# Kernel tuning notes

Measured on AMD Instinct MI355X. Metric: run time of the kernel, lower is better.

Reference implementation:

```python
import jax, jax.numpy as jnp
import numpy as np

N_NODES = 50000
N_EDGES = 800000
IN_DIM = 64
OUT_DIM = 64
HID = OUT_DIM // 2  # 32
N_LAYERS = 9  # layer_num; layer_num >= 7 => no temporal conv, conv dropout unused


def _layernorm(x, w, b, eps=1e-5):
    mu = jnp.mean(x, axis=-1, keepdims=True)
    var = jnp.var(x, axis=-1, keepdims=True)
    return (x - mu) * jax.lax.rsqrt(var + eps) * w + b


def _conv(x, Wp, Wn, Ws, src, tgt, pos_m, neg_m):
    # relation-wise gather -> linear -> masked merge -> single scatter_add
    xs = x[src]  # [E, d_in]
    m = jnp.where(pos_m[:, None], xs @ Wp.T, 0.0) + jnp.where(neg_m[:, None], xs @ Wn.T, 0.0)
    agg = jax.ops.segment_sum(m, tgt, num_segments=N_NODES)
    return agg + x @ Ws.T


def _asfr(x, ln_w, ln_b, gw, gb):
    xn = _layernorm(x, ln_w, ln_b)
    w = jax.nn.sigmoid(xn @ gw.T + gb)
    w1 = jnp.where(w > 0.5, 1.0, w)
    w2 = jnp.where(w > 0.5, 0.0, w)
    x1 = w1 * x
    x2 = w2 * x
    h = x.shape[1] // 2
    return jnp.concatenate([x1[:, :h] + x2[:, h:], x1[:, h:] + x2[:, :h]], axis=1)


def setup_inputs() -> dict:
    key = jax.random.key(0)
    ks = jax.random.split(key, 24)
    init_emb = jax.random.normal(ks[0], (N_NODES, IN_DIM), dtype=jnp.float32)
    src = jax.random.randint(ks[1], (N_EDGES,), 0, N_NODES)
    tgt = jax.random.randint(ks[2], (N_EDGES,), 0, N_NODES)
    sign = jnp.where(jax.random.uniform(ks[3], (N_EDGES,)) > 0.5, 1, -1).astype(jnp.int64)
    edge_index_s = jnp.stack([src, tgt, sign], axis=1).astype(jnp.int64)

    def w(k, shape, fan_in):
        return jax.random.normal(k, shape, dtype=jnp.float32) * (1.0 / np.sqrt(fan_in))

    inp = dict(init_emb=init_emb, edge_index_s=edge_index_s)
    # conv1: in 64 -> 32, relations pos/neg + self loop (no bias)
    inp["W1_pos"] = w(ks[4], (HID, IN_DIM), IN_DIM)
    inp["W1_neg"] = w(ks[5], (HID, IN_DIM), IN_DIM)
    inp["W1_self"] = w(ks[6], (HID, IN_DIM), IN_DIM)
    # 8 further convs: 32 -> 32, stacked
    L = N_LAYERS - 1
    inp["Wl_pos"] = w(ks[7], (L, HID, HID), HID)
    inp["Wl_neg"] = w(ks[8], (L, HID, HID), HID)
    inp["Wl_self"] = w(ks[9], (L, HID, HID), HID)
    # ASFR
    inp["asfr_ln_w"] = jnp.ones((HID,), jnp.float32)
    inp["asfr_ln_b"] = jnp.zeros((HID,), jnp.float32)
    inp["asfr_gate_w"] = w(ks[10], (HID, HID), HID)
    inp["asfr_gate_b"] = jnp.zeros((HID,), jnp.float32)
    # projection 32 -> 64
    inp["proj_w"] = w(ks[11], (OUT_DIM, HID), HID)
    inp["proj_b"] = jnp.zeros((OUT_DIM,), jnp.float32)
    # readout MLP: 64 -> 64 -> 64 -> 1, layernorm + relu between
    inp["mlp_w1"] = w(ks[12], (OUT_DIM, OUT_DIM), OUT_DIM)
    inp["mlp_b1"] = jnp.zeros((OUT_DIM,), jnp.float32)
    inp["mlp_ln1_w"] = jnp.ones((OUT_DIM,), jnp.float32)
    inp["mlp_ln1_b"] = jnp.zeros((OUT_DIM,), jnp.float32)
    inp["mlp_w2"] = w(ks[13], (OUT_DIM, OUT_DIM), OUT_DIM)
    inp["mlp_b2"] = jnp.zeros((OUT_DIM,), jnp.float32)
    inp["mlp_ln2_w"] = jnp.ones((OUT_DIM,), jnp.float32)
    inp["mlp_ln2_b"] = jnp.zeros((OUT_DIM,), jnp.float32)
    inp["mlp_w3"] = w(ks[14], (1, OUT_DIM), OUT_DIM)
    inp["mlp_b3"] = jnp.zeros((1,), jnp.float32)
    return inp


def reference(init_emb, edge_index_s, W1_pos, W1_neg, W1_self, Wl_pos, Wl_neg, Wl_self,
              asfr_ln_w, asfr_ln_b, asfr_gate_w, asfr_gate_b, proj_w, proj_b,
              mlp_w1, mlp_b1, mlp_ln1_w, mlp_ln1_b, mlp_w2, mlp_b2,
              mlp_ln2_w, mlp_ln2_b, mlp_w3, mlp_b3):
    src = edge_index_s[:, 0]
    tgt = edge_index_s[:, 1]
    sign = edge_index_s[:, 2]
    pos_m = sign > 0
    neg_m = sign < 0

    z = jax.nn.elu(_conv(init_emb, W1_pos, W1_neg, W1_self, src, tgt, pos_m, neg_m))
    z = _asfr(z, asfr_ln_w, asfr_ln_b, asfr_gate_w, asfr_gate_b)
    for i in range(Wl_pos.shape[0]):
        z_new = jax.nn.elu(_conv(z, Wl_pos[i], Wl_neg[i], Wl_self[i], src, tgt, pos_m, neg_m))
        z = z_new if i == 0 else z_new + 0.1 * z
    z = jax.nn.elu(z @ proj_w.T + proj_b)
    # readout MLP (eval mode: dropout identity)
    h = jax.nn.relu(_layernorm(z @ mlp_w1.T + mlp_b1, mlp_ln1_w, mlp_ln1_b))
    h = jax.nn.relu(_layernorm(h @ mlp_w2.T + mlp_b2, mlp_ln2_w, mlp_ln2_b))
    prob = jax.nn.sigmoid(h @ mlp_w3.T + mlp_b3)
    return (z, prob)
```

## Files before the change

kernel.cpp:

```cpp
#include <hip/hip_runtime.h>
#include <hip/hip_bf16.h>

#define NODES 50000
#define EDGES 800000

__device__ __forceinline__ float elu1(float x) { return x > 0.f ? x : expm1f(x); }

union F4 { float4 v; float f[4]; };

__global__ __launch_bounds__(256) void k_hist(const int* __restrict__ ei, int* __restrict__ deg) {
  int e = blockIdx.x * 256 + threadIdx.x;
  if (e < EDGES) atomicAdd(deg + ei[e * 3 + 1], 1);
}

__global__ __launch_bounds__(512) void k_scan1(const int* __restrict__ deg, int* __restrict__ offs,
                                               int* __restrict__ bsum) {
  __shared__ int s[512];
  int t = threadIdx.x, i = blockIdx.x * 512 + t;
  int v = (i < NODES) ? deg[i] : 0;
  s[t] = v;
  __syncthreads();
  for (int o = 1; o < 512; o <<= 1) {
    int x = (t >= o) ? s[t - o] : 0;
    __syncthreads();
    s[t] += x;
    __syncthreads();
  }
  if (i < NODES) offs[i] = s[t] - v;
  if (t == 511) bsum[blockIdx.x] = s[511];
}

__global__ __launch_bounds__(128) void k_scan2(int* __restrict__ bsum, int nb) {
  __shared__ int s[128];
  int t = threadIdx.x;
  int v = (t < nb) ? bsum[t] : 0;
  s[t] = v;
  __syncthreads();
  for (int o = 1; o < 128; o <<= 1) {
    int x = (t >= o) ? s[t - o] : 0;
    __syncthreads();
    s[t] += x;
    __syncthreads();
  }
  if (t < nb) bsum[t] = s[t] - v;
}

__global__ __launch_bounds__(512) void k_scan3(int* __restrict__ offs, const int* __restrict__ bsum,
                                               int* __restrict__ cursor) {
  int i = blockIdx.x * 512 + threadIdx.x;
  if (i < NODES) {
    int v = offs[i] + bsum[blockIdx.x];
    offs[i] = v;
    cursor[i] = v;
  }
  if (i == 0) offs[NODES] = EDGES;
}

__global__ __launch_bounds__(256) void k_scatter(const int* __restrict__ ei, int* __restrict__ cursor,
                                                 unsigned* __restrict__ perm) {
  int e = blockIdx.x * 256 + threadIdx.x;
  if (e >= EDGES) return;
  int src = ei[e * 3 + 0];
  int tgt = ei[e * 3 + 1];
  int sg  = ei[e * 3 + 2];
  int p = atomicAdd(cursor + tgt, 1);
  perm[p] = (unsigned)src | (sg < 0 ? 0x80000000u : 0u);
}

__global__ __launch_bounds__(256) void k_lin64(const float* __restrict__ x,
    const float* __restrict__ Wp, const float* __restrict__ Wn, const float* __restrict__ Ws,
    __hip_bfloat16* __restrict__ ypb, __hip_bfloat16* __restrict__ ynb, float* __restrict__ ys) {
  constexpr int K4 = 16;
  __shared__ float4 wp[K4][32], wn[K4][32], wsm[K4][32];
  __shared__ float4 xs[8][K4];
  for (int i = threadIdx.x; i < 32 * K4; i += 256) {
    int k4 = i >> 5, c = i & 31;
    wp[k4][c]  = ((const float4*)Wp)[c * K4 + k4];
    wn[k4][c]  = ((const float4*)Wn)[c * K4 + k4];
    wsm[k4][c] = ((const float4*)Ws)[c * K4 + k4];
  }
  int base = blockIdx.x * 8;
  for (int i = threadIdx.x; i < 8 * K4; i += 256) {
    int r = i / K4, k4 = i - r * K4;
    xs[r][k4] = ((const float4*)(x + (size_t)(base + r) * 64))[k4];
  }
  __syncthreads();
  int lane = threadIdx.x & 31, local = threadIdx.x >> 5;
  float ap = 0.f, an = 0.f, asf = 0.f;
#pragma unroll
  for (int k4 = 0; k4 < K4; k4++) {
    float4 xv = xs[local][k4];
    float4 a = wp[k4][lane], b = wn[k4][lane], c = wsm[k4][lane];
    ap  = fmaf(xv.w, a.w, fmaf(xv.z, a.z, fmaf(xv.y, a.y, fmaf(xv.x, a.x, ap))));
    an  = fmaf(xv.w, b.w, fmaf(xv.z, b.z, fmaf(xv.y, b.y, fmaf(xv.x, b.x, an))));
    asf = fmaf(xv.w, c.w, fmaf(xv.z, c.z, fmaf(xv.y, c.y, fmaf(xv.x, c.x, asf))));
  }
  size_t o = (size_t)(base + local) * 32 + lane;
  ypb[o] = __float2bfloat16(ap);
  ynb[o] = __float2bfloat16(an);
  ys[o] = asf;
}

template <int DO_ASFR, int DO_RES, int DO_LIN, int WRITE_Z>
__global__ __launch_bounds__(256) void k_layer(
    const unsigned short* __restrict__ ypi, const unsigned short* __restrict__ yni,
    float* __restrict__ ys,
    const unsigned* __restrict__ perm, const int* __restrict__ offs,
    float* __restrict__ z,
    const float* __restrict__ lnw, const float* __restrict__ lnb,
    const float* __restrict__ gw, const float* __restrict__ gb,
    const float* __restrict__ Wp, const float* __restrict__ Wn, const float* __restrict__ Ws,
    __hip_bfloat16* __restrict__ ypo, __hip_bfloat16* __restrict__ yno) {
  __shared__ float4 wps[8][32], wns[8][32], wss[8][32], gws[8][32];
  __shared__ float zrow[8][36], xrow[8][36];
  int t = threadIdx.x;
  if (DO_LIN) {
    int k4 = t >> 5, c = t & 31;
    wps[k4][c] = ((const float4*)Wp)[c * 8 + k4];
    wns[k4][c] = ((const float4*)Wn)[c * 8 + k4];
    wss[k4][c] = ((const float4*)Ws)[c * 8 + k4];
    if (DO_ASFR) gws[k4][c] = ((const float4*)gw)[c * 8 + k4];
  }
  int lane = t & 31, local = t >> 5;
  int node = blockIdx.x * 8 + local;
  int es = lane >> 2, fs = lane & 3;
  int beg = offs[node], end = offs[node + 1];
  float a[8];
#pragma unroll
  for (int i = 0; i < 8; i++) a[i] = 0.f;
#pragma unroll 2
  for (int b = beg + es; b < end; b += 8) {
    unsigned u = perm[b];
    const unsigned short* base = (u >> 31) ? yni : ypi;
    uint4 v = *((const uint4*)(base + (size_t)(u & 0x7FFFFFFFu) * 32) + fs);
    a[0] += __uint_as_float(v.x << 16);
    a[1] += __uint_as_float(v.x & 0xffff0000u);
    a[2] += __uint_as_float(v.y << 16);
    a[3] += __uint_as_float(v.y & 0xffff0000u);
    a[4] += __uint_as_float(v.z << 16);
    a[5] += __uint_as_float(v.z & 0xffff0000u);
    a[6] += __uint_as_float(v.w << 16);
    a[7] += __uint_as_float(v.w & 0xffff0000u);
  }
#pragma unroll
  for (int m = 4; m <= 16; m <<= 1) {
#pragma unroll
    for (int i = 0; i < 8; i++) a[i] += __shfl_xor(a[i], m, 32);
  }
  if (es == 0) {
    const float* ysr = ys + (size_t)node * 32 + fs * 8;
    F4 s0, s1;
    s0.v = *(const float4*)ysr;
    s1.v = *(const float4*)(ysr + 4);
    float o[8];
#pragma unroll
    for (int i = 0; i < 4; i++) o[i] = elu1(a[i] + s0.f[i]);
#pragma unroll
    for (int i = 0; i < 4; i++) o[4 + i] = elu1(a[4 + i] + s1.f[i]);
    if (DO_RES) {
      const float* rr = z + (size_t)node * 32 + fs * 8;
      F4 r0, r1;
      r0.v = *(const float4*)rr;
      r1.v = *(const float4*)(rr + 4);
#pragma unroll
      for (int i = 0; i < 4; i++) { o[i] += 0.1f * r0.f[i]; o[4 + i] += 0.1f * r1.f[i]; }
    }
#pragma unroll
    for (int i = 0; i < 8; i++) zrow[local][fs * 8 + i] = o[i];
    if (WRITE_Z) {
      float* zw = z + (size_t)node * 32 + fs * 8;
      *(float4*)zw = make_float4(o[0], o[1], o[2], o[3]);
      *(float4*)(zw + 4) = make_float4(o[4], o[5], o[6], o[7]);
    }
  }
  __syncthreads();
  if (!DO_LIN) return;
  if (DO_ASFR) {
    float v = zrow[local][lane];
    float s = v;
#pragma unroll
    for (int m = 16; m; m >>= 1) s += __shfl_xor(s, m, 32);
    float mu = s * (1.f / 32.f);
    float d = v - mu, sq = d * d;
#pragma unroll
    for (int m = 16; m; m >>= 1) sq += __shfl_xor(sq, m, 32);
    float xn = d * rsqrtf(sq * (1.f / 32.f) + 1e-5f) * lnw[lane] + lnb[lane];
    xrow[local][lane] = xn;
    float ga = gb[lane];
#pragma unroll
    for (int k4 = 0; k4 < 8; k4++) {
      float4 xv = *((const float4*)&xrow[local][0] + k4);
      float4 w = gws[k4][lane];
      ga = fmaf(xv.w, w.w, fmaf(xv.z, w.z, fmaf(xv.y, w.y, fmaf(xv.x, w.x, ga))));
    }
    float g = 1.f / (1.f + __expf(-ga));
    float w1 = g > 0.5f ? 1.f : g;
    float w2 = g > 0.5f ? 0.f : g;
    float zn = w1 * v + __shfl_xor(w2 * v, 16, 32);
    zrow[local][lane] = zn;
  }
  float ap = 0.f, an = 0.f, asf = 0.f;
#pragma unroll
  for (int k4 = 0; k4 < 8; k4++) {
    float4 xv = *((const float4*)&zrow[local][0] + k4);
    float4 a2 = wps[k4][lane], b2 = wns[k4][lane], c2 = wss[k4][lane];
    ap  = fmaf(xv.w, a2.w, fmaf(xv.z, a2.z, fmaf(xv.y, a2.y, fmaf(xv.x, a2.x, ap))));
    an  = fmaf(xv.w, b2.w, fmaf(xv.z, b2.z, fmaf(xv.y, b2.y, fmaf(xv.x, b2.x, an))));
    asf = fmaf(xv.w, c2.w, fmaf(xv.z, c2.z, fmaf(xv.y, c2.y, fmaf(xv.x, c2.x, asf))));
  }
  size_t o = (size_t)node * 32 + lane;
  ypo[o] = __float2bfloat16(ap);
  yno[o] = __float2bfloat16(an);
  ys[o] = asf;
}

__global__ __launch_bounds__(256) void k_mlp(const float* __restrict__ z,
    const float* __restrict__ pw, const float* __restrict__ pb,
    const float* __restrict__ w1, const float* __restrict__ b1,
    const float* __restrict__ l1w, const float* __restrict__ l1b,
    const float* __restrict__ w2, const float* __restrict__ b2,
    const float* __restrict__ l2w, const float* __restrict__ l2b,
    const float* __restrict__ w3, const float* __restrict__ b3,
    float* __restrict__ outz, float* __restrict__ outp) {
  __shared__ float4 pT4[32 * 16];
  __shared__ float4 w1T4[64 * 16], w2T4[64 * 16];
  __shared__ float4 hbuf4[64 * 17];
  __shared__ float pb_s[64], b1_s[64], l1w_s[64], l1b_s[64], b2_s[64], l2w_s[64], l2b_s[64], w3_s[64];
  int t = threadIdx.x;
  for (int i = t; i < 512; i += 256) {
    int k = i >> 4, j4 = i & 15;
    float4 v;
    v.x = pw[(j4 * 4 + 0) * 32 + k]; v.y = pw[(j4 * 4 + 1) * 32 + k];
    v.z = pw[(j4 * 4 + 2) * 32 + k]; v.w = pw[(j4 * 4 + 3) * 32 + k];
    pT4[i] = v;
  }
  for (int i = t; i < 1024; i += 256) {
    int k = i >> 4, j4 = i & 15;
    float4 v, u;
    v.x = w1[(j4 * 4 + 0) * 64 + k]; v.y = w1[(j4 * 4 + 1) * 64 + k];
    v.z = w1[(j4 * 4 + 2) * 64 + k]; v.w = w1[(j4 * 4 + 3) * 64 + k];
    u.x = w2[(j4 * 4 + 0) * 64 + k]; u.y = w2[(j4 * 4 + 1) * 64 + k];
    u.z = w2[(j4 * 4 + 2) * 64 + k]; u.w = w2[(j4 * 4 + 3) * 64 + k];
    w1T4[i] = v; w2T4[i] = u;
  }
  if (t < 64) {
    pb_s[t] = pb[t]; b1_s[t] = b1[t]; l1w_s[t] = l1w[t]; l1b_s[t] = l1b[t];
    b2_s[t] = b2[t]; l2w_s[t] = l2w[t]; l2b_s[t] = l2b[t]; w3_s[t] = w3[t];
  }
  __syncthreads();
  int g = t >> 2, q = t & 3;
  int node = blockIdx.x * 64 + g;
  if (node >= NODES) return;
  float bb3 = b3[0];
  {
    const float4* z4 = (const float4*)(z + (size_t)node * 32);
    hbuf4[g * 17 + q * 2 + 0] = z4[q * 2 + 0];
    hbuf4[g * 17 + q * 2 + 1] = z4[q * 2 + 1];
  }
  float acc[16], h[16];
#pragma unroll
  for (int i = 0; i < 16; i++) acc[i] = pb_s[q * 16 + i];
#pragma unroll 2
  for (int k4 = 0; k4 < 8; k4++) {
    F4 hv; hv.v = hbuf4[g * 17 + k4];
#pragma unroll
    for (int c = 0; c < 4; c++) {
      float hk = hv.f[c];
      const float4* wrow = &pT4[(k4 * 4 + c) * 16 + q * 4];
#pragma unroll
      for (int j4 = 0; j4 < 4; j4++) {
        float4 w = wrow[j4];
        acc[j4 * 4 + 0] = fmaf(hk, w.x, acc[j4 * 4 + 0]);
        acc[j4 * 4 + 1] = fmaf(hk, w.y, acc[j4 * 4 + 1]);
        acc[j4 * 4 + 2] = fmaf(hk, w.z, acc[j4 * 4 + 2]);
        acc[j4 * 4 + 3] = fmaf(hk, w.w, acc[j4 * 4 + 3]);
      }
    }
  }
#pragma unroll
  for (int i = 0; i < 16; i++) h[i] = elu1(acc[i]);
  {
    float4* oz = (float4*)(outz + (size_t)node * 64 + q * 16);
#pragma unroll
    for (int i4 = 0; i4 < 4; i4++)
      oz[i4] = make_float4(h[i4 * 4], h[i4 * 4 + 1], h[i4 * 4 + 2], h[i4 * 4 + 3]);
#pragma unroll
    for (int i4 = 0; i4 < 4; i4++)
      hbuf4[g * 17 + q * 4 + i4] = make_float4(h[i4 * 4], h[i4 * 4 + 1], h[i4 * 4 + 2], h[i4 * 4 + 3]);
  }
#pragma unroll
  for (int i = 0; i < 16; i++) acc[i] = b1_s[q * 16 + i];
#pragma unroll 2
  for (int k4 = 0; k4 < 16; k4++) {
    F4 hv; hv.v = hbuf4[g * 17 + k4];
#pragma unroll
    for (int c = 0; c < 4; c++) {
      float hk = hv.f[c];
      const float4* wrow = &w1T4[(k4 * 4 + c) * 16 + q * 4];
#pragma unroll
      for (int j4 = 0; j4 < 4; j4++) {
        float4 w = wrow[j4];
        acc[j4 * 4 + 0] = fmaf(hk, w.x, acc[j4 * 4 + 0]);
        acc[j4 * 4 + 1] = fmaf(hk, w.y, acc[j4 * 4 + 1]);
        acc[j4 * 4 + 2] = fmaf(hk, w.z, acc[j4 * 4 + 2]);
        acc[j4 * 4 + 3] = fmaf(hk, w.w, acc[j4 * 4 + 3]);
      }
    }
  }
  {
    float s = 0.f;
#pragma unroll
    for (int i = 0; i < 16; i++) s += acc[i];
    s += __shfl_xor(s, 1, 4); s += __shfl_xor(s, 2, 4);
    float mu = s * (1.f / 64.f);
    float vs = 0.f;
#pragma unroll
    for (int i = 0; i < 16; i++) { float dd = acc[i] - mu; vs += dd * dd; }
    vs += __shfl_xor(vs, 1, 4); vs += __shfl_xor(vs, 2, 4);
    float rs = rsqrtf(vs * (1.f / 64.f) + 1e-5f);
#pragma unroll
    for (int i = 0; i < 16; i++)
      h[i] = fmaxf((acc[i] - mu) * rs * l1w_s[q * 16 + i] + l1b_s[q * 16 + i], 0.f);
  }
#pragma unroll
  for (int i4 = 0; i4 < 4; i4++)
    hbuf4[g * 17 + q * 4 + i4] = make_float4(h[i4 * 4], h[i4 * 4 + 1], h[i4 * 4 + 2], h[i4 * 4 + 3]);
#pragma unroll
  for (int i = 0; i < 16; i++) acc[i] = b2_s[q * 16 + i];
#pragma unroll 2
  for (int k4 = 0; k4 < 16; k4++) {
    F4 hv; hv.v = hbuf4[g * 17 + k4];
#pragma unroll
    for (int c = 0; c < 4; c++) {
      float hk = hv.f[c];
      const float4* wrow = &w2T4[(k4 * 4 + c) * 16 + q * 4];
#pragma unroll
      for (int j4 = 0; j4 < 4; j4++) {
        float4 w = wrow[j4];
        acc[j4 * 4 + 0] = fmaf(hk, w.x, acc[j4 * 4 + 0]);
        acc[j4 * 4 + 1] = fmaf(hk, w.y, acc[j4 * 4 + 1]);
        acc[j4 * 4 + 2] = fmaf(hk, w.z, acc[j4 * 4 + 2]);
        acc[j4 * 4 + 3] = fmaf(hk, w.w, acc[j4 * 4 + 3]);
      }
    }
  }
  {
    float s = 0.f;
#pragma unroll
    for (int i = 0; i < 16; i++) s += acc[i];
    s += __shfl_xor(s, 1, 4); s += __shfl_xor(s, 2, 4);
    float mu = s * (1.f / 64.f);
    float vs = 0.f;
#pragma unroll
    for (int i = 0; i < 16; i++) { float dd = acc[i] - mu; vs += dd * dd; }
    vs += __shfl_xor(vs, 1, 4); vs += __shfl_xor(vs, 2, 4);
    float rs = rsqrtf(vs * (1.f / 64.f) + 1e-5f);
    float p = 0.f;
#pragma unroll
    for (int i = 0; i < 16; i++) {
      float hv2 = fmaxf((acc[i] - mu) * rs * l2w_s[q * 16 + i] + l2b_s[q * 16 + i], 0.f);
      p = fmaf(hv2, w3_s[q * 16 + i], p);
    }
    p += __shfl_xor(p, 1, 4); p += __shfl_xor(p, 2, 4);
    if (q == 0) outp[node] = 1.f / (1.f + __expf(-(p + bb3)));
  }
}

extern "C" void kernel_launch(void* const* d_in, const int* in_sizes, int n_in,
                              void* d_out, int out_size, void* d_ws, size_t ws_size,
                              hipStream_t stream) {
  const float* init_emb = (const float*)d_in[0];
  const int*   ei  = (const int*)d_in[1];
  const float* W1p = (const float*)d_in[2];
  const float* W1n = (const float*)d_in[3];
  const float* W1s = (const float*)d_in[4];
  const float* Wlp = (const float*)d_in[5];
  const float* Wln = (const float*)d_in[6];
  const float* Wls = (const float*)d_in[7];
  const float* lnw = (const float*)d_in[8];
  const float* lnb = (const float*)d_in[9];
  const float* gw  = (const float*)d_in[10];
  const float* gb  = (const float*)d_in[11];
  const float* pw  = (const float*)d_in[12];
  const float* pb  = (const float*)d_in[13];
  const float* w1  = (const float*)d_in[14];
  const float* b1  = (const float*)d_in[15];
  const float* l1w = (const float*)d_in[16];
  const float* l1b = (const float*)d_in[17];
  const float* w2  = (const float*)d_in[18];
  const float* b2  = (const float*)d_in[19];
  const float* l2w = (const float*)d_in[20];
  const float* l2b = (const float*)d_in[21];
  const float* w3  = (const float*)d_in[22];
  const float* b3  = (const float*)d_in[23];

  char* ws = (char*)d_ws;
  size_t off = 0;
  auto alloc = [&](size_t b) { void* p = ws + off; off = (off + b + 255) & ~(size_t)255; return p; };
  __hip_bfloat16* ypA = (__hip_bfloat16*)alloc(NODES * 32 * 2);
  __hip_bfloat16* ynA = (__hip_bfloat16*)alloc(NODES * 32 * 2);
  __hip_bfloat16* ypB = (__hip_bfloat16*)alloc(NODES * 32 * 2);
  __hip_bfloat16* ynB = (__hip_bfloat16*)alloc(NODES * 32 * 2);
  float*    ysel   = (float*)alloc(NODES * 32 * 4);
  float*    zbuf   = (float*)alloc(NODES * 32 * 4);
  unsigned* perm   = (unsigned*)alloc(EDGES * 4);
  int*      deg    = (int*)alloc(NODES * 4);
  int*      offs   = (int*)alloc((NODES + 1) * 4);
  int*      cursor = (int*)alloc(NODES * 4);
  int*      bsum   = (int*)alloc(128 * 4);

  hipMemsetAsync(deg, 0, NODES * 4, stream);
  k_hist<<<(EDGES + 255) / 256, 256, 0, stream>>>(ei, deg);
  int nb = (NODES + 511) / 512;
  k_scan1<<<nb, 512, 0, stream>>>(deg, offs, bsum);
  k_scan2<<<1, 128, 0, stream>>>(bsum, nb);
  k_scan3<<<nb, 512, 0, stream>>>(offs, bsum, cursor);
  k_scatter<<<(EDGES + 255) / 256, 256, 0, stream>>>(ei, cursor, perm);

  const int G = NODES / 8;
  k_lin64<<<G, 256, 0, stream>>>(init_emb, W1p, W1n, W1s, ypA, ynA, ysel);
  k_layer<1, 0, 1, 0><<<G, 256, 0, stream>>>((const unsigned short*)ypA, (const unsigned short*)ynA,
      ysel, perm, offs, zbuf, lnw, lnb, gw, gb, Wlp, Wln, Wls, ypB, ynB);
  k_layer<0, 0, 1, 1><<<G, 256, 0, stream>>>((const unsigned short*)ypB, (const unsigned short*)ynB,
      ysel, perm, offs, zbuf, nullptr, nullptr, nullptr, nullptr,
      Wlp + 1024, Wln + 1024, Wls + 1024, ypA, ynA);
  const __hip_bfloat16* yin_p = ypA; const __hip_bfloat16* yin_n = ynA;
  __hip_bfloat16* yout_p = ypB; __hip_bfloat16* yout_n = ynB;
  for (int i = 1; i < 7; i++) {
    k_layer<0, 1, 1, 1><<<G, 256, 0, stream>>>((const unsigned short*)yin_p, (const unsigned short*)yin_n,
        ysel, perm, offs, zbuf, nullptr, nullptr, nullptr, nullptr,
        Wlp + (i + 1) * 1024, Wln + (i + 1) * 1024, Wls + (i + 1) * 1024, yout_p, yout_n);
    const __hip_bfloat16* tp = yin_p; const __hip_bfloat16* tn = yin_n;
    yin_p = yout_p; yin_n = yout_n;
    yout_p = (__hip_bfloat16*)tp; yout_n = (__hip_bfloat16*)tn;
  }
  k_layer<0, 1, 0, 1><<<G, 256, 0, stream>>>((const unsigned short*)yin_p, (const unsigned short*)yin_n,
      ysel, perm, offs, zbuf, nullptr, nullptr, nullptr, nullptr,
      nullptr, nullptr, nullptr, nullptr, nullptr);

  float* outz = (float*)d_out;
  float* outp = outz + (size_t)NODES * 64;
  k_mlp<<<(NODES * 4 + 255) / 256, 256, 0, stream>>>(zbuf, pw, pb, w1, b1, l1w, l1b,
                                                     w2, b2, l2w, l2b, w3, b3, outz, outp);
}
```

Before: 407.5 us.

## Two-pass bucketed CSR build and dual-accumulator edge gather loop

The CSR construction now bins edges by 256-node target bucket before scattering. Block-local shared-memory atomics replace the global per-node cursor atomics, so the final scatter into perm stays within a bucket's region. The binned staging array reuses the ypA buffer before k_lin64 overwrites it. The per-node aggregation loop also processes two edges per iteration with separate accumulators to increase memory-level parallelism. The cost is extra kernel launches and an extra pass over the edge list.

```diff
diff --git a/kernel.cpp b/kernel.cpp
--- a/kernel.cpp
+++ b/kernel.cpp
@@ -3,14 +3,33 @@
 
 #define NODES 50000
 #define EDGES 800000
+#define BSH 8
+#define NBUCK 196
+#define NBIN_BLOCKS 391
 
 __device__ __forceinline__ float elu1(float x) { return x > 0.f ? x : expm1f(x); }
 
 union F4 { float4 v; float f[4]; };
 
-__global__ __launch_bounds__(256) void k_hist(const int* __restrict__ ei, int* __restrict__ deg) {
-  int e = blockIdx.x * 256 + threadIdx.x;
-  if (e < EDGES) atomicAdd(deg + ei[e * 3 + 1], 1);
+__global__ __launch_bounds__(256) void k_hist2(const int* __restrict__ ei, int* __restrict__ deg,
+                                               int* __restrict__ bucket_cnt) {
+  __shared__ int cnt[NBUCK];
+  int t = threadIdx.x;
+  for (int i = t; i < NBUCK; i += 256) cnt[i] = 0;
+  __syncthreads();
+  int base = blockIdx.x * 2048;
+#pragma unroll
+  for (int i = 0; i < 8; i++) {
+    int e = base + i * 256 + t;
+    if (e < EDGES) {
+      int tgt = ei[e * 3 + 1];
+      atomicAdd(deg + tgt, 1);
+      atomicAdd(&cnt[tgt >> BSH], 1);
+    }
+  }
+  __syncthreads();
+  for (int i = t; i < NBUCK; i += 256)
+    if (cnt[i]) atomicAdd(bucket_cnt + i, cnt[i]);
 }
 
 __global__ __launch_bounds__(512) void k_scan1(const int* __restrict__ deg, int* __restrict__ offs,
@@ -45,26 +64,80 @@
   if (t < nb) bsum[t] = s[t] - v;
 }
 
-__global__ __launch_bounds__(512) void k_scan3(int* __restrict__ offs, const int* __restrict__ bsum,
-                                               int* __restrict__ cursor) {
+__global__ __launch_bounds__(512) void k_scan3(int* __restrict__ offs, const int* __restrict__ bsum) {
   int i = blockIdx.x * 512 + threadIdx.x;
-  if (i < NODES) {
-    int v = offs[i] + bsum[blockIdx.x];
-    offs[i] = v;
-    cursor[i] = v;
-  }
+  if (i < NODES) offs[i] += bsum[blockIdx.x];
   if (i == 0) offs[NODES] = EDGES;
 }
 
-__global__ __launch_bounds__(256) void k_scatter(const int* __restrict__ ei, int* __restrict__ cursor,
-                                                 unsigned* __restrict__ perm) {
-  int e = blockIdx.x * 256 + threadIdx.x;
-  if (e >= EDGES) return;
-  int src = ei[e * 3 + 0];
-  int tgt = ei[e * 3 + 1];
-  int sg  = ei[e * 3 + 2];
-  int p = atomicAdd(cursor + tgt, 1);
-  perm[p] = (unsigned)src | (sg < 0 ? 0x80000000u : 0u);
+__global__ __launch_bounds__(256) void k_bscan(const int* __restrict__ bucket_cnt,
+                                               int* __restrict__ bucket_base,
+                                               int* __restrict__ bucket_cursor) {
+  __shared__ int s[256];
+  int t = threadIdx.x;
+  int v = (t < NBUCK) ? bucket_cnt[t] : 0;
+  s[t] = v;
+  __syncthreads();
+  for (int o = 1; o < 256; o <<= 1) {
+    int x = (t >= o) ? s[t - o] : 0;
+    __syncthreads();
+    s[t] += x;
+    __syncthreads();
+  }
+  if (t < NBUCK) { int e = s[t] - v; bucket_base[t] = e; bucket_cursor[t] = e; }
+}
+
+__global__ __launch_bounds__(256) void k_bin(const int* __restrict__ ei,
+                                             int* __restrict__ bucket_cursor,
+                                             uint2* __restrict__ binned) {
+  __shared__ int cnt[NBUCK], base[NBUCK];
+  int t = threadIdx.x;
+  for (int i = t; i < NBUCK; i += 256) cnt[i] = 0;
+  __syncthreads();
+  int eb = blockIdx.x * 2048;
+#pragma unroll
+  for (int i = 0; i < 8; i++) {
+    int e = eb + i * 256 + t;
+    if (e < EDGES) atomicAdd(&cnt[ei[e * 3 + 1] >> BSH], 1);
+  }
+  __syncthreads();
+  for (int i = t; i < NBUCK; i += 256) {
+    int c = cnt[i];
+    base[i] = c ? atomicAdd(bucket_cursor + i, c) : 0;
+    cnt[i] = 0;
+  }
+  __syncthreads();
+#pragma unroll
+  for (int i = 0; i < 8; i++) {
+    int e = eb + i * 256 + t;
+    if (e < EDGES) {
+      int src = ei[e * 3 + 0];
+      int tgt = ei[e * 3 + 1];
+      int sg  = ei[e * 3 + 2];
+      unsigned val = (unsigned)src | (sg < 0 ? 0x80000000u : 0u);
+      int bkt = tgt >> BSH;
+      int r = atomicAdd(&cnt[bkt], 1);
+      binned[base[bkt] + r] = make_uint2(val, (unsigned)tgt);
+    }
+  }
+}
+
+__global__ __launch_bounds__(256) void k_scatter2(const uint2* __restrict__ binned,
+                                                  const int* __restrict__ bucket_base,
+                                                  const int* __restrict__ bucket_cnt,
+                                                  const int* __restrict__ offs,
+                                                  unsigned* __restrict__ perm) {
+  __shared__ int cur[256];
+  int b = blockIdx.x, t = threadIdx.x;
+  int t0 = b << BSH;
+  cur[t] = (t0 + t < NODES) ? offs[t0 + t] : 0;
+  __syncthreads();
+  int n = bucket_cnt[b], bb = bucket_base[b];
+  for (int i = t; i < n; i += 256) {
+    uint2 e = binned[bb + i];
+    int p = atomicAdd(&cur[e.y - t0], 1);
+    perm[p] = e.x;
+  }
 }
 
 __global__ __launch_bounds__(256) void k_lin64(const float* __restrict__ x,
@@ -100,6 +173,16 @@
   ynb[o] = __float2bfloat16(an);
   ys[o] = asf;
 }
+
+#define ACC8(A, V)                                   \
+  A[0] += __uint_as_float((V).x << 16);              \
+  A[1] += __uint_as_float((V).x & 0xffff0000u);      \
+  A[2] += __uint_as_float((V).y << 16);              \
+  A[3] += __uint_as_float((V).y & 0xffff0000u);      \
+  A[4] += __uint_as_float((V).z << 16);              \
+  A[5] += __uint_as_float((V).z & 0xffff0000u);      \
+  A[6] += __uint_as_float((V).w << 16);              \
+  A[7] += __uint_as_float((V).w & 0xffff0000u);
 
 template <int DO_ASFR, int DO_RES, int DO_LIN, int WRITE_Z>
 __global__ __launch_bounds__(256) void k_layer(
@@ -125,27 +208,32 @@
   int node = blockIdx.x * 8 + local;
   int es = lane >> 2, fs = lane & 3;
   int beg = offs[node], end = offs[node + 1];
-  float a[8];
-#pragma unroll
-  for (int i = 0; i < 8; i++) a[i] = 0.f;
-#pragma unroll 2
-  for (int b = beg + es; b < end; b += 8) {
-    unsigned u = perm[b];
-    const unsigned short* base = (u >> 31) ? yni : ypi;
-    uint4 v = *((const uint4*)(base + (size_t)(u & 0x7FFFFFFFu) * 32) + fs);
-    a[0] += __uint_as_float(v.x << 16);
-    a[1] += __uint_as_float(v.x & 0xffff0000u);
-    a[2] += __uint_as_float(v.y << 16);
-    a[3] += __uint_as_float(v.y & 0xffff0000u);
-    a[4] += __uint_as_float(v.z << 16);
-    a[5] += __uint_as_float(v.z & 0xffff0000u);
-    a[6] += __uint_as_float(v.w << 16);
-    a[7] += __uint_as_float(v.w & 0xffff0000u);
-  }
+  float a0[8], a1[8];
+#pragma unroll
+  for (int i = 0; i < 8; i++) { a0[i] = 0.f; a1[i] = 0.f; }
+  int b = beg + es;
+  for (; b + 8 < end; b += 16) {
+    unsigned u0 = perm[b];
+    unsigned u1 = perm[b + 8];
+    const unsigned short* p0 = (u0 >> 31) ? yni : ypi;
+    const unsigned short* p1 = (u1 >> 31) ? yni : ypi;
+    uint4 v0 = *((const uint4*)(p0 + (size_t)(u0 & 0x7FFFFFFFu) * 32) + fs);
+    uint4 v1 = *((const uint4*)(p1 + (size_t)(u1 & 0x7FFFFFFFu) * 32) + fs);
+    ACC8(a0, v0);
+    ACC8(a1, v1);
+  }
+  if (b < end) {
+    unsigned u0 = perm[b];
+    const unsigned short* p0 = (u0 >> 31) ? yni : ypi;
+    uint4 v0 = *((const uint4*)(p0 + (size_t)(u0 & 0x7FFFFFFFu) * 32) + fs);
+    ACC8(a0, v0);
+  }
+#pragma unroll
+  for (int i = 0; i < 8; i++) a0[i] += a1[i];
 #pragma unroll
   for (int m = 4; m <= 16; m <<= 1) {
 #pragma unroll
-    for (int i = 0; i < 8; i++) a[i] += __shfl_xor(a[i], m, 32);
+    for (int i = 0; i < 8; i++) a0[i] += __shfl_xor(a0[i], m, 32);
   }
   if (es == 0) {
     const float* ysr = ys + (size_t)node * 32 + fs * 8;
@@ -154,9 +242,9 @@
     s1.v = *(const float4*)(ysr + 4);
     float o[8];
 #pragma unroll
-    for (int i = 0; i < 4; i++) o[i] = elu1(a[i] + s0.f[i]);
-#pragma unroll
-    for (int i = 0; i < 4; i++) o[4 + i] = elu1(a[4 + i] + s1.f[i]);
+    for (int i = 0; i < 4; i++) o[i] = elu1(a0[i] + s0.f[i]);
+#pragma unroll
+    for (int i = 0; i < 4; i++) o[4 + i] = elu1(a0[4 + i] + s1.f[i]);
     if (DO_RES) {
       const float* rr = z + (size_t)node * 32 + fs * 8;
       F4 r0, r1;
@@ -406,16 +494,22 @@
   unsigned* perm   = (unsigned*)alloc(EDGES * 4);
   int*      deg    = (int*)alloc(NODES * 4);
   int*      offs   = (int*)alloc((NODES + 1) * 4);
-  int*      cursor = (int*)alloc(NODES * 4);
   int*      bsum   = (int*)alloc(128 * 4);
+  int*      bucket_cnt    = (int*)alloc(NBUCK * 4);
+  int*      bucket_base   = (int*)alloc(NBUCK * 4);
+  int*      bucket_cursor = (int*)alloc(NBUCK * 4);
+  uint2*    binned = (uint2*)ypA;
 
   hipMemsetAsync(deg, 0, NODES * 4, stream);
-  k_hist<<<(EDGES + 255) / 256, 256, 0, stream>>>(ei, deg);
+  hipMemsetAsync(bucket_cnt, 0, NBUCK * 4, stream);
+  k_hist2<<<NBIN_BLOCKS, 256, 0, stream>>>(ei, deg, bucket_cnt);
   int nb = (NODES + 511) / 512;
   k_scan1<<<nb, 512, 0, stream>>>(deg, offs, bsum);
   k_scan2<<<1, 128, 0, stream>>>(bsum, nb);
-  k_scan3<<<nb, 512, 0, stream>>>(offs, bsum, cursor);
-  k_scatter<<<(EDGES + 255) / 256, 256, 0, stream>>>(ei, cursor, perm);
+  k_scan3<<<nb, 512, 0, stream>>>(offs, bsum);
+  k_bscan<<<1, 256, 0, stream>>>(bucket_cnt, bucket_base, bucket_cursor);
+  k_bin<<<NBIN_BLOCKS, 256, 0, stream>>>(ei, bucket_cursor, binned);
+  k_scatter2<<<NBUCK, 256, 0, stream>>>(binned, bucket_base, bucket_cnt, offs, perm);
 
   const int G = NODES / 8;
   k_lin64<<<G, 256, 0, stream>>>(init_emb, W1p, W1n, W1s, ypA, ynA, ysel);
```

New measurement: 395.7 us. 1.03x faster.
